# Kernel tuning notes

Hardware: AMD Instinct MI355X
Metric: run time of the kernel (lower is better)

Reference implementation:

```python
import jax, jax.numpy as jnp
import numpy as np

N, E = 50000, 1600000
NODE_F, EDGE_F = 128, 64
H, F = 4, 16
NEG_SLOPE = 0.2


def setup_inputs() -> dict:
    key = jax.random.key(0)
    ks = jax.random.split(key, 12)
    return {
        "nfeat": jax.random.normal(ks[0], (N, NODE_F), jnp.float32),
        "efeat": jax.random.normal(ks[1], (E, EDGE_F), jnp.float32),
        "W_node": jax.random.normal(ks[2], (NODE_F, H * F), jnp.float32) * 0.1,
        "b_node": jax.random.normal(ks[3], (H * F,), jnp.float32) * 0.1,
        "W_edge": jax.random.normal(ks[4], (EDGE_F, H * F), jnp.float32) * 0.1,
        "b_edge": jax.random.normal(ks[5], (H * F,), jnp.float32) * 0.1,
        "attn_l": jax.random.normal(ks[6], (H, F), jnp.float32) * 0.1,
        "attn_r": jax.random.normal(ks[7], (H, F), jnp.float32) * 0.1,
        "attn_e": jax.random.normal(ks[8], (H, F), jnp.float32) * 0.1,
        "src": jax.random.randint(ks[9], (E,), 0, N, jnp.int32),
        "dst": jax.random.randint(ks[10], (E,), 0, N, jnp.int32),
    }


def reference(nfeat, efeat, W_node, b_node, W_edge, b_edge,
              attn_l, attn_r, attn_e, src, dst):
    n = nfeat.shape[0]
    node_feat = (nfeat @ W_node + b_node).reshape(n, H, F)   # [N,H,F]
    edge_feat = (efeat @ W_edge + b_edge).reshape(-1, H, F)  # [E,H,F]
    el = jnp.einsum('nhf,hf->nh', node_feat, attn_l)  # [N,H]
    er = jnp.einsum('nhf,hf->nh', node_feat, attn_r)  # [N,H]
    ee = jnp.einsum('ehf,hf->eh', edge_feat, attn_e)  # [E,H]
    el_prime = el[src] + ee                            # u_add_e, [E,H]
    e = el_prime + er[dst]                             # e_add_v, [E,H]
    e = jnp.where(e > 0, e, NEG_SLOPE * e)             # leaky_relu
    # edge softmax over incoming edges per destination node
    emax = jax.ops.segment_max(e, dst, num_segments=n)      # [N,H]
    ex = jnp.exp(e - emax[dst])                              # [E,H]
    denom = jax.ops.segment_sum(ex, dst, num_segments=n)    # [N,H]
    a = ex / denom[dst]                                      # [E,H]
    # msg_fn: a * el_prime (scalar per edge/head) -> scatter-sum to dst
    m = a * el_prime                                          # [E,H]
    rst = jax.ops.segment_sum(m, dst, num_segments=n)        # [N,H]
    return rst[..., None]                                     # [N,H,1]
```

## Files before the change

### kernel.cpp

```cpp
#include <hip/hip_runtime.h>
#include <hip/hip_fp16.h>

constexpr int H = 4;
constexpr int F = 16;
constexpr int NODE_F = 128;
constexpr int EDGE_F = 64;
constexpr float NEG_SLOPE = 0.2f;

__global__ void fold_kernel(const float* __restrict__ Wn, const float* __restrict__ bn,
                            const float* __restrict__ Wed, const float* __restrict__ bed,
                            const float* __restrict__ al, const float* __restrict__ ar,
                            const float* __restrict__ ae,
                            float* __restrict__ Wl, float* __restrict__ Wr,
                            float* __restrict__ We, float* __restrict__ bv,
                            int* __restrict__ total) {
    int idx = threadIdx.x;
    if (idx == 0) *total = 0;
    if (idx < NODE_F * H) {
        int k = idx >> 2, h = idx & 3;
        float sl = 0.f, sr = 0.f;
        #pragma unroll
        for (int f = 0; f < F; ++f) {
            float w = Wn[k * (H * F) + h * F + f];
            sl += w * al[h * F + f];
            sr += w * ar[h * F + f];
        }
        Wl[idx] = sl; Wr[idx] = sr;
    }
    if (idx < EDGE_F * H) {
        int k = idx >> 2, h = idx & 3;
        float s = 0.f;
        #pragma unroll
        for (int f = 0; f < F; ++f) s += Wed[k * (H * F) + h * F + f] * ae[h * F + f];
        We[idx] = s;
    }
    if (idx < H) {
        float sl = 0.f, sr = 0.f, se = 0.f;
        #pragma unroll
        for (int f = 0; f < F; ++f) {
            sl += bn[idx * F + f] * al[idx * F + f];
            sr += bn[idx * F + f] * ar[idx * F + f];
            se += bed[idx * F + f] * ae[idx * F + f];
        }
        bv[idx] = sl; bv[H + idx] = sr; bv[2 * H + idx] = se;
    }
}

__global__ void node_proj_kernel(const float* __restrict__ nfeat,
                                 const float* __restrict__ Wl, const float* __restrict__ Wr,
                                 const float* __restrict__ bv,
                                 float* __restrict__ el, float* __restrict__ er,
                                 int* __restrict__ deg, int N) {
    __shared__ float sWl[NODE_F * H];
    __shared__ float sWr[NODE_F * H];
    for (int i = threadIdx.x; i < NODE_F * H; i += blockDim.x) { sWl[i] = Wl[i]; sWr[i] = Wr[i]; }
    __syncthreads();
    int lane = threadIdx.x & 63;
    int wave = (int)(((size_t)blockIdx.x * blockDim.x + threadIdx.x) >> 6);
    int sub = lane & 3, ln = lane >> 2;
    int n = wave * 16 + ln;
    if (n >= N) return;
    float accl[H] = {0.f, 0.f, 0.f, 0.f};
    float accr[H] = {0.f, 0.f, 0.f, 0.f};
    const float4* row = (const float4*)(nfeat + (size_t)n * NODE_F);
    #pragma unroll
    for (int i = 0; i < 8; ++i) {
        float4 v = row[sub + 4 * i];
        int k0 = (sub + 4 * i) * 4;
        float vv[4] = {v.x, v.y, v.z, v.w};
        #pragma unroll
        for (int j = 0; j < 4; ++j) {
            float4 wl = *(const float4*)&sWl[(k0 + j) * H];
            float4 wr = *(const float4*)&sWr[(k0 + j) * H];
            accl[0] += vv[j] * wl.x; accl[1] += vv[j] * wl.y;
            accl[2] += vv[j] * wl.z; accl[3] += vv[j] * wl.w;
            accr[0] += vv[j] * wr.x; accr[1] += vv[j] * wr.y;
            accr[2] += vv[j] * wr.z; accr[3] += vv[j] * wr.w;
        }
    }
    #pragma unroll
    for (int m = 1; m < 4; m <<= 1) {
        #pragma unroll
        for (int h = 0; h < H; ++h) {
            accl[h] += __shfl_xor(accl[h], m);
            accr[h] += __shfl_xor(accr[h], m);
        }
    }
    el[(size_t)n * H + sub] = accl[sub] + bv[sub];
    er[(size_t)n * H + sub] = accr[sub] + bv[H + sub];
    if (sub == 0) deg[n] = 0;
}

__global__ void edge_proj_kernel(const float* __restrict__ efeat,
                                 const int* __restrict__ src, const int* __restrict__ dst,
                                 const float* __restrict__ We, const float* __restrict__ bv,
                                 const float* __restrict__ el,
                                 uint2* __restrict__ pay, unsigned short* __restrict__ idx,
                                 int* __restrict__ deg, int E) {
    __shared__ float sWe[EDGE_F * H];
    __shared__ float sbe[H];
    for (int i = threadIdx.x; i < EDGE_F * H; i += blockDim.x) sWe[i] = We[i];
    if (threadIdx.x < H) sbe[threadIdx.x] = bv[2 * H + threadIdx.x];
    __syncthreads();
    int lane = threadIdx.x & 63;
    int wave = (int)(((size_t)blockIdx.x * blockDim.x + threadIdx.x) >> 6);
    int sub = lane & 3, le = lane >> 2;
    int e = wave * 16 + le;
    if (e >= E) return;
    float acc[H] = {0.f, 0.f, 0.f, 0.f};
    const float4* row = (const float4*)(efeat + (size_t)e * EDGE_F);
    #pragma unroll
    for (int i = 0; i < 4; ++i) {
        float4 v = row[sub + 4 * i];
        int k0 = (sub + 4 * i) * 4;
        float vv[4] = {v.x, v.y, v.z, v.w};
        #pragma unroll
        for (int j = 0; j < 4; ++j) {
            float4 w = *(const float4*)&sWe[(k0 + j) * H];
            acc[0] += vv[j] * w.x; acc[1] += vv[j] * w.y;
            acc[2] += vv[j] * w.z; acc[3] += vv[j] * w.w;
        }
    }
    #pragma unroll
    for (int m = 1; m < 4; m <<= 1) {
        #pragma unroll
        for (int h = 0; h < H; ++h) acc[h] += __shfl_xor(acc[h], m);
    }
    if (sub == 0) {
        int s = src[e];
        float4 elv = *(const float4*)(el + (size_t)s * H);
        float p0 = elv.x + acc[0] + sbe[0];
        float p1 = elv.y + acc[1] + sbe[1];
        float p2 = elv.z + acc[2] + sbe[2];
        float p3 = elv.w + acc[3] + sbe[3];
        __half2 a = __floats2half2_rn(p0, p1);
        __half2 b = __floats2half2_rn(p2, p3);
        uint2 w;
        w.x = *(unsigned int*)&a;
        w.y = *(unsigned int*)&b;
        pay[e] = w;
        idx[e] = (unsigned short)atomicAdd(deg + dst[e], 1);
    }
}

__global__ void offsets_kernel(const int* __restrict__ deg, int* __restrict__ off,
                               int* __restrict__ total, int N) {
    int lane = threadIdx.x & 63;
    int gid = blockIdx.x * blockDim.x + threadIdx.x;
    int x = (gid < N) ? deg[gid] : 0;
    int incl = x;
    #pragma unroll
    for (int s = 1; s < 64; s <<= 1) {
        int y = __shfl_up(incl, s);
        if (lane >= s) incl += y;
    }
    int wtot = __shfl(incl, 63);
    int base = 0;
    if (lane == 63) base = atomicAdd(total, wtot);
    base = __shfl(base, 63);
    if (gid < N) off[gid] = base + incl - x;
}

__global__ void scatter_eid_kernel(const int* __restrict__ dst,
                                   const unsigned short* __restrict__ idx,
                                   const int* __restrict__ off, int* __restrict__ eid, int E) {
    int e = blockIdx.x * blockDim.x + threadIdx.x;
    if (e >= E) return;
    eid[off[dst[e]] + (int)idx[e]] = e;
}

__global__ void node_reduce_kernel(const uint2* __restrict__ pay,
                                   const int* __restrict__ eid,
                                   const int* __restrict__ off, const int* __restrict__ deg,
                                   const float* __restrict__ er,
                                   float* __restrict__ out, int N) {
    int lane = threadIdx.x & 63;
    int wave = (int)(((size_t)blockIdx.x * blockDim.x + threadIdx.x) >> 6);
    int g = lane >> 4;
    int gl = lane & 15;
    int n = wave * 4 + g;
    if (n >= N) return;
    int o = off[n], dg = deg[n];
    float4 erv = *(const float4*)(er + (size_t)n * H);
    float n0 = 0.f, n1 = 0.f, n2 = 0.f, n3 = 0.f;
    float d0 = 0.f, d1 = 0.f, d2 = 0.f, d3 = 0.f;
    for (int i = gl; i < dg; i += 16) {
        uint2 w = pay[eid[o + i]];
        float2 f01 = __half22float2(*(const __half2*)&w.x);
        float2 f23 = __half22float2(*(const __half2*)&w.y);
        float e0 = f01.x + erv.x, e1 = f01.y + erv.y, e2 = f23.x + erv.z, e3 = f23.y + erv.w;
        e0 = e0 > 0.f ? e0 : NEG_SLOPE * e0;
        e1 = e1 > 0.f ? e1 : NEG_SLOPE * e1;
        e2 = e2 > 0.f ? e2 : NEG_SLOPE * e2;
        e3 = e3 > 0.f ? e3 : NEG_SLOPE * e3;
        float x0 = __expf(e0), x1 = __expf(e1), x2 = __expf(e2), x3 = __expf(e3);
        n0 += x0 * f01.x; n1 += x1 * f01.y; n2 += x2 * f23.x; n3 += x3 * f23.y;
        d0 += x0; d1 += x1; d2 += x2; d3 += x3;
    }
    #pragma unroll
    for (int s = 8; s; s >>= 1) {
        n0 += __shfl_down(n0, s, 16); n1 += __shfl_down(n1, s, 16);
        n2 += __shfl_down(n2, s, 16); n3 += __shfl_down(n3, s, 16);
        d0 += __shfl_down(d0, s, 16); d1 += __shfl_down(d1, s, 16);
        d2 += __shfl_down(d2, s, 16); d3 += __shfl_down(d3, s, 16);
    }
    if (gl == 0) {
        *(float4*)(out + (size_t)n * H) =
            make_float4(d0 > 0.f ? n0 / d0 : 0.f, d1 > 0.f ? n1 / d1 : 0.f,
                        d2 > 0.f ? n2 / d2 : 0.f, d3 > 0.f ? n3 / d3 : 0.f);
    }
}

__global__ void node_proj_fb_kernel(const float* __restrict__ nfeat,
                                    const float* __restrict__ Wl, const float* __restrict__ Wr,
                                    const float* __restrict__ bv,
                                    float* __restrict__ el, float* __restrict__ er,
                                    float* __restrict__ num, float* __restrict__ den, int N) {
    __shared__ float sWl[NODE_F * H];
    __shared__ float sWr[NODE_F * H];
    for (int i = threadIdx.x; i < NODE_F * H; i += blockDim.x) { sWl[i] = Wl[i]; sWr[i] = Wr[i]; }
    __syncthreads();
    int n = blockIdx.x * blockDim.x + threadIdx.x;
    if (n >= N) return;
    float accl[H] = {0.f, 0.f, 0.f, 0.f};
    float accr[H] = {0.f, 0.f, 0.f, 0.f};
    const float4* row = (const float4*)(nfeat + (size_t)n * NODE_F);
    #pragma unroll
    for (int j = 0; j < NODE_F / 4; ++j) {
        float4 v = row[j];
        #pragma unroll
        for (int h = 0; h < H; ++h) {
            accl[h] += v.x * sWl[(4 * j + 0) * H + h] + v.y * sWl[(4 * j + 1) * H + h]
                     + v.z * sWl[(4 * j + 2) * H + h] + v.w * sWl[(4 * j + 3) * H + h];
            accr[h] += v.x * sWr[(4 * j + 0) * H + h] + v.y * sWr[(4 * j + 1) * H + h]
                     + v.z * sWr[(4 * j + 2) * H + h] + v.w * sWr[(4 * j + 3) * H + h];
        }
    }
    size_t base = (size_t)n * H;
    #pragma unroll
    for (int h = 0; h < H; ++h) {
        el[base + h] = accl[h] + bv[h];
        er[base + h] = accr[h] + bv[H + h];
        num[base + h] = 0.f;
        den[base + h] = 0.f;
    }
}

__global__ void edge_atomic_kernel(const float* __restrict__ efeat,
                                   const int* __restrict__ src, const int* __restrict__ dst,
                                   const float* __restrict__ We, const float* __restrict__ bv,
                                   const float* __restrict__ el, const float* __restrict__ er,
                                   float* __restrict__ num, float* __restrict__ den, int E) {
    __shared__ float sWe[EDGE_F * H];
    __shared__ float sbe[H];
    for (int i = threadIdx.x; i < EDGE_F * H; i += blockDim.x) sWe[i] = We[i];
    if (threadIdx.x < H) sbe[threadIdx.x] = bv[2 * H + threadIdx.x];
    __syncthreads();
    int e = blockIdx.x * blockDim.x + threadIdx.x;
    if (e >= E) return;
    float acc[H] = {sbe[0], sbe[1], sbe[2], sbe[3]};
    const float4* row = (const float4*)(efeat + (size_t)e * EDGE_F);
    #pragma unroll
    for (int j = 0; j < EDGE_F / 4; ++j) {
        float4 v = row[j];
        #pragma unroll
        for (int h = 0; h < H; ++h) {
            acc[h] += v.x * sWe[(4 * j + 0) * H + h] + v.y * sWe[(4 * j + 1) * H + h]
                    + v.z * sWe[(4 * j + 2) * H + h] + v.w * sWe[(4 * j + 3) * H + h];
        }
    }
    int s = src[e], d = dst[e];
    float4 elv = *(const float4*)(el + (size_t)s * H);
    float4 erv = *(const float4*)(er + (size_t)d * H);
    float p0 = elv.x + acc[0], p1 = elv.y + acc[1], p2 = elv.z + acc[2], p3 = elv.w + acc[3];
    float e0 = p0 + erv.x, e1 = p1 + erv.y, e2 = p2 + erv.z, e3 = p3 + erv.w;
    e0 = e0 > 0.f ? e0 : NEG_SLOPE * e0;
    e1 = e1 > 0.f ? e1 : NEG_SLOPE * e1;
    e2 = e2 > 0.f ? e2 : NEG_SLOPE * e2;
    e3 = e3 > 0.f ? e3 : NEG_SLOPE * e3;
    float x0 = __expf(e0), x1 = __expf(e1), x2 = __expf(e2), x3 = __expf(e3);
    float* nb = num + (size_t)d * H;
    float* db = den + (size_t)d * H;
    atomicAdd(nb + 0, x0 * p0); atomicAdd(nb + 1, x1 * p1);
    atomicAdd(nb + 2, x2 * p2); atomicAdd(nb + 3, x3 * p3);
    atomicAdd(db + 0, x0); atomicAdd(db + 1, x1);
    atomicAdd(db + 2, x2); atomicAdd(db + 3, x3);
}

__global__ void finalize_kernel(const float* __restrict__ num, const float* __restrict__ den,
                                float* __restrict__ out, int NH) {
    int i = blockIdx.x * blockDim.x + threadIdx.x;
    if (i < NH) {
        float d = den[i];
        out[i] = d > 0.f ? num[i] / d : 0.f;
    }
}

extern "C" void kernel_launch(void* const* d_in, const int* in_sizes, int n_in,
                              void* d_out, int out_size, void* d_ws, size_t ws_size,
                              hipStream_t stream) {
    const float* nfeat = (const float*)d_in[0];
    const float* efeat = (const float*)d_in[1];
    const float* Wn    = (const float*)d_in[2];
    const float* bn    = (const float*)d_in[3];
    const float* Wed   = (const float*)d_in[4];
    const float* bed   = (const float*)d_in[5];
    const float* al    = (const float*)d_in[6];
    const float* ar    = (const float*)d_in[7];
    const float* ae    = (const float*)d_in[8];
    const int*   src   = (const int*)d_in[9];
    const int*   dst   = (const int*)d_in[10];

    int N = in_sizes[0] / NODE_F;
    int E = in_sizes[1] / EDGE_F;
    float* out = (float*)d_out;
    float* ws  = (float*)d_ws;

    size_t p_pay  = 0;
    size_t p_el   = p_pay + (size_t)E * 2;
    size_t p_er   = p_el + (size_t)N * H;
    size_t p_Wl   = p_er + (size_t)N * H;
    size_t p_Wr   = p_Wl + 512;
    size_t p_We   = p_Wr + 512;
    size_t p_bv   = p_We + 256;
    size_t p_tot  = p_bv + 16;
    size_t p_deg  = p_tot + 16;
    size_t p_off  = p_deg + (size_t)N;
    size_t p_idx  = p_off + (size_t)N;
    size_t p_eid  = p_idx + ((size_t)E / 2 + 8);
    size_t csr_total = (p_eid + (size_t)E) * sizeof(float);

    if (ws_size >= csr_total) {
        uint2* pay = (uint2*)(ws + p_pay);
        float* el  = ws + p_el;
        float* er  = ws + p_er;
        float* Wl  = ws + p_Wl;
        float* Wr  = ws + p_Wr;
        float* We  = ws + p_We;
        float* bv  = ws + p_bv;
        int* total = (int*)(ws + p_tot);
        int* deg   = (int*)(ws + p_deg);
        int* off   = (int*)(ws + p_off);
        unsigned short* idx = (unsigned short*)(ws + p_idx);
        int* eid   = (int*)(ws + p_eid);

        fold_kernel<<<1, 512, 0, stream>>>(Wn, bn, Wed, bed, al, ar, ae, Wl, Wr, We, bv, total);
        node_proj_kernel<<<(int)(((size_t)N * 4 + 255) / 256), 256, 0, stream>>>(
            nfeat, Wl, Wr, bv, el, er, deg, N);
        edge_proj_kernel<<<(int)(((size_t)E * 4 + 255) / 256), 256, 0, stream>>>(
            efeat, src, dst, We, bv, el, pay, idx, deg, E);
        offsets_kernel<<<(N + 255) / 256, 256, 0, stream>>>(deg, off, total, N);
        scatter_eid_kernel<<<(E + 255) / 256, 256, 0, stream>>>(dst, idx, off, eid, E);
        node_reduce_kernel<<<(int)(((size_t)N * 16 + 255) / 256), 256, 0, stream>>>(
            pay, eid, off, deg, er, out, N);
    } else {
        float* el  = ws;
        float* er  = el + (size_t)N * H;
        float* num = er + (size_t)N * H;
        float* den = num + (size_t)N * H;
        float* Wl  = den + (size_t)N * H;
        float* Wr  = Wl + 512;
        float* We  = Wr + 512;
        float* bv  = We + 256;
        int* total = (int*)(bv + 16);

        fold_kernel<<<1, 512, 0, stream>>>(Wn, bn, Wed, bed, al, ar, ae, Wl, Wr, We, bv, total);
        node_proj_fb_kernel<<<(N + 255) / 256, 256, 0, stream>>>(nfeat, Wl, Wr, bv,
                                                                 el, er, num, den, N);
        edge_atomic_kernel<<<(E + 255) / 256, 256, 0, stream>>>(efeat, src, dst, We, bv,
                                                                el, er, num, den, E);
        finalize_kernel<<<(N * H + 255) / 256, 256, 0, stream>>>(num, den, out, N * H);
    }
}
```

Measured before the change: 175.0 us.

## Build CSR histogram before edge projection and scatter edge ids in-place

The in-degree histogram over dst now runs in extra blocks appended to the node projection launch, and deg zeroing moves into the fold kernel. Offsets are computed before the edge projection, which claims a slot with a second atomic on a per-node cursor and writes eid directly. This removes the separate scatter_eid kernel and the per-edge 16-bit idx array. The cost is a second pass of atomics over all edges and a single-block zeroing loop over N. In the fallback path the fold kernel also zeroes N ints placed after total, which may run past the smaller workspace.

```diff
diff --git a/kernel.cpp b/kernel.cpp
--- a/kernel.cpp
+++ b/kernel.cpp
@@ -13,9 +13,10 @@
                             const float* __restrict__ ae,
                             float* __restrict__ Wl, float* __restrict__ Wr,
                             float* __restrict__ We, float* __restrict__ bv,
-                            int* __restrict__ total) {
+                            int* __restrict__ total, int* __restrict__ deg, int N) {
     int idx = threadIdx.x;
     if (idx == 0) *total = 0;
+    for (int i = idx; i < N; i += 512) deg[i] = 0;
     if (idx < NODE_F * H) {
         int k = idx >> 2, h = idx & 3;
         float sl = 0.f, sr = 0.f;
@@ -46,11 +47,17 @@
     }
 }
 
-__global__ void node_proj_kernel(const float* __restrict__ nfeat,
+__global__ void node_hist_kernel(const float* __restrict__ nfeat,
                                  const float* __restrict__ Wl, const float* __restrict__ Wr,
                                  const float* __restrict__ bv,
+                                 const int* __restrict__ dst,
                                  float* __restrict__ el, float* __restrict__ er,
-                                 int* __restrict__ deg, int N) {
+                                 int* __restrict__ deg, int N, int E, int Nb) {
+    if ((int)blockIdx.x >= Nb) {
+        int e = ((int)blockIdx.x - Nb) * blockDim.x + threadIdx.x;
+        if (e < E) atomicAdd(deg + dst[e], 1);
+        return;
+    }
     __shared__ float sWl[NODE_F * H];
     __shared__ float sWr[NODE_F * H];
     for (int i = threadIdx.x; i < NODE_F * H; i += blockDim.x) { sWl[i] = Wl[i]; sWr[i] = Wr[i]; }
@@ -88,15 +95,32 @@
     }
     el[(size_t)n * H + sub] = accl[sub] + bv[sub];
     er[(size_t)n * H + sub] = accr[sub] + bv[H + sub];
-    if (sub == 0) deg[n] = 0;
+}
+
+__global__ void offsets_kernel(const int* __restrict__ deg, int* __restrict__ off,
+                               int* __restrict__ cur, int* __restrict__ total, int N) {
+    int lane = threadIdx.x & 63;
+    int gid = blockIdx.x * blockDim.x + threadIdx.x;
+    int x = (gid < N) ? deg[gid] : 0;
+    int incl = x;
+    #pragma unroll
+    for (int s = 1; s < 64; s <<= 1) {
+        int y = __shfl_up(incl, s);
+        if (lane >= s) incl += y;
+    }
+    int wtot = __shfl(incl, 63);
+    int base = 0;
+    if (lane == 63) base = atomicAdd(total, wtot);
+    base = __shfl(base, 63);
+    if (gid < N) { off[gid] = base + incl - x; cur[gid] = 0; }
 }
 
 __global__ void edge_proj_kernel(const float* __restrict__ efeat,
                                  const int* __restrict__ src, const int* __restrict__ dst,
                                  const float* __restrict__ We, const float* __restrict__ bv,
                                  const float* __restrict__ el,
-                                 uint2* __restrict__ pay, unsigned short* __restrict__ idx,
-                                 int* __restrict__ deg, int E) {
+                                 const int* __restrict__ off, int* __restrict__ cur,
+                                 uint2* __restrict__ pay, int* __restrict__ eid, int E) {
     __shared__ float sWe[EDGE_F * H];
     __shared__ float sbe[H];
     for (int i = threadIdx.x; i < EDGE_F * H; i += blockDim.x) sWe[i] = We[i];
@@ -127,46 +151,21 @@
         for (int h = 0; h < H; ++h) acc[h] += __shfl_xor(acc[h], m);
     }
     if (sub == 0) {
-        int s = src[e];
+        int s = src[e], d = dst[e];
         float4 elv = *(const float4*)(el + (size_t)s * H);
         float p0 = elv.x + acc[0] + sbe[0];
         float p1 = elv.y + acc[1] + sbe[1];
         float p2 = elv.z + acc[2] + sbe[2];
         float p3 = elv.w + acc[3] + sbe[3];
-        __half2 a = __floats2half2_rn(p0, p1);
-        __half2 b = __floats2half2_rn(p2, p3);
+        __half2 ha = __floats2half2_rn(p0, p1);
+        __half2 hb = __floats2half2_rn(p2, p3);
         uint2 w;
-        w.x = *(unsigned int*)&a;
-        w.y = *(unsigned int*)&b;
+        w.x = *(unsigned int*)&ha;
+        w.y = *(unsigned int*)&hb;
         pay[e] = w;
-        idx[e] = (unsigned short)atomicAdd(deg + dst[e], 1);
-    }
-}
-
-__global__ void offsets_kernel(const int* __restrict__ deg, int* __restrict__ off,
-                               int* __restrict__ total, int N) {
-    int lane = threadIdx.x & 63;
-    int gid = blockIdx.x * blockDim.x + threadIdx.x;
-    int x = (gid < N) ? deg[gid] : 0;
-    int incl = x;
-    #pragma unroll
-    for (int s = 1; s < 64; s <<= 1) {
-        int y = __shfl_up(incl, s);
-        if (lane >= s) incl += y;
-    }
-    int wtot = __shfl(incl, 63);
-    int base = 0;
-    if (lane == 63) base = atomicAdd(total, wtot);
-    base = __shfl(base, 63);
-    if (gid < N) off[gid] = base + incl - x;
-}
-
-__global__ void scatter_eid_kernel(const int* __restrict__ dst,
-                                   const unsigned short* __restrict__ idx,
-                                   const int* __restrict__ off, int* __restrict__ eid, int E) {
-    int e = blockIdx.x * blockDim.x + threadIdx.x;
-    if (e >= E) return;
-    eid[off[dst[e]] + (int)idx[e]] = e;
+        int slot = atomicAdd(cur + d, 1);
+        eid[off[d] + slot] = e;
+    }
 }
 
 __global__ void node_reduce_kernel(const uint2* __restrict__ pay,
@@ -326,8 +325,8 @@
     size_t p_tot  = p_bv + 16;
     size_t p_deg  = p_tot + 16;
     size_t p_off  = p_deg + (size_t)N;
-    size_t p_idx  = p_off + (size_t)N;
-    size_t p_eid  = p_idx + ((size_t)E / 2 + 8);
+    size_t p_cur  = p_off + (size_t)N;
+    size_t p_eid  = p_cur + (size_t)N;
     size_t csr_total = (p_eid + (size_t)E) * sizeof(float);
 
     if (ws_size >= csr_total) {
@@ -341,16 +340,19 @@
         int* total = (int*)(ws + p_tot);
         int* deg   = (int*)(ws + p_deg);
         int* off   = (int*)(ws + p_off);
-        unsigned short* idx = (unsigned short*)(ws + p_idx);
+        int* cur   = (int*)(ws + p_cur);
         int* eid   = (int*)(ws + p_eid);
 
-        fold_kernel<<<1, 512, 0, stream>>>(Wn, bn, Wed, bed, al, ar, ae, Wl, Wr, We, bv, total);
-        node_proj_kernel<<<(int)(((size_t)N * 4 + 255) / 256), 256, 0, stream>>>(
-            nfeat, Wl, Wr, bv, el, er, deg, N);
+        int Nb = (int)(((size_t)N * 4 + 255) / 256);
+        int Eb = (E + 255) / 256;
+
+        fold_kernel<<<1, 512, 0, stream>>>(Wn, bn, Wed, bed, al, ar, ae,
+                                           Wl, Wr, We, bv, total, deg, N);
+        node_hist_kernel<<<Nb + Eb, 256, 0, stream>>>(nfeat, Wl, Wr, bv, dst,
+                                                      el, er, deg, N, E, Nb);
+        offsets_kernel<<<(N + 255) / 256, 256, 0, stream>>>(deg, off, cur, total, N);
         edge_proj_kernel<<<(int)(((size_t)E * 4 + 255) / 256), 256, 0, stream>>>(
-            efeat, src, dst, We, bv, el, pay, idx, deg, E);
-        offsets_kernel<<<(N + 255) / 256, 256, 0, stream>>>(deg, off, total, N);
-        scatter_eid_kernel<<<(E + 255) / 256, 256, 0, stream>>>(dst, idx, off, eid, E);
+            efeat, src, dst, We, bv, el, off, cur, pay, eid, E);
         node_reduce_kernel<<<(int)(((size_t)N * 16 + 255) / 256), 256, 0, stream>>>(
             pay, eid, off, deg, er, out, N);
     } else {
@@ -363,8 +365,10 @@
         float* We  = Wr + 512;
         float* bv  = We + 256;
         int* total = (int*)(bv + 16);
-
-        fold_kernel<<<1, 512, 0, stream>>>(Wn, bn, Wed, bed, al, ar, ae, Wl, Wr, We, bv, total);
+        int* degf  = total + 16;
+
+        fold_kernel<<<1, 512, 0, stream>>>(Wn, bn, Wed, bed, al, ar, ae,
+                                           Wl, Wr, We, bv, total, degf, N);
         node_proj_fb_kernel<<<(N + 255) / 256, 256, 0, stream>>>(nfeat, Wl, Wr, bv,
                                                                  el, er, num, den, N);
         edge_atomic_kernel<<<(E + 255) / 256, 256, 0, stream>>>(efeat, src, dst, We, bv,
```

New measurement: 237.7 us. 1.36x slower.
